# Optimization experiments

Hardware: AMD Instinct MI355X
Metric: run time of the kernel (lower is better)

## Reference

```python
import jax, jax.numpy as jnp
import numpy as np

B, N, M, R = 128, 511, 256, 64
IN = 512  # word_dim + tag_dim


def setup_inputs() -> dict:
    key = jax.random.key(0)
    ks = jax.random.split(key, 16)
    def w(k, shape, fan_in):
        return jax.random.normal(k, shape, dtype=jnp.float32) / np.sqrt(fan_in)
    inp = {
        "word_tag_emb": jax.random.normal(ks[0], (B, N, IN), dtype=jnp.float32),
        "rel_emb": jax.random.normal(ks[1], (B, N, R), dtype=jnp.float32),
        "n_nodes": N,
    }
    for j, nm in enumerate(["ix", "fx", "ux", "ox"]):
        inp["W" + nm] = w(ks[2 + j], (IN, M), IN)
        inp["b" + nm] = jnp.zeros((M,), jnp.float32)
    for j, nm in enumerate(["ih", "fh", "uh", "oh"]):
        inp["W" + nm] = w(ks[6 + j], (M, M), M)
        inp["b" + nm] = jnp.zeros((M,), jnp.float32)
    # seq_lstm (nn.LSTM, 1 layer): gate order i, f, g, o; stored [in, 4M]
    inp["W_seq_ih"] = w(ks[10], (M + R, 4 * M), M + R)
    inp["W_seq_hh"] = w(ks[11], (M, 4 * M), M)
    inp["b_seq_ih"] = jnp.zeros((4 * M,), jnp.float32)
    inp["b_seq_hh"] = jnp.zeros((4 * M,), jnp.float32)
    return inp


def reference(word_tag_emb, rel_emb,
              Wix, bix, Wfx, bfx, Wux, bux, Wox, box,
              Wih, bih, Wfh, bfh, Wuh, buh, Woh, boh,
              W_seq_ih, W_seq_hh, b_seq_ih, b_seq_hh, n_nodes):
    Bn, Nn, _ = word_tag_emb.shape
    Mm = Wih.shape[0]
    dt = word_tag_emb.dtype

    def lstm_cell(x, h, c):
        g = x @ W_seq_ih + h @ W_seq_hh + (b_seq_ih + b_seq_hh)
        i, f, gg, o = jnp.split(g, 4, axis=-1)
        c2 = jax.nn.sigmoid(f) * c + jax.nn.sigmoid(i) * jnp.tanh(gg)
        return jax.nn.sigmoid(o) * jnp.tanh(c2), c2

    def step(carry, node):
        h_buf, c_buf = carry  # [B, N, M] state buffers
        ch = jnp.stack([2 * node + 1, 2 * node + 2])        # heap children
        valid = (ch < Nn).astype(dt)[:, None, None]          # [2,1,1]
        idx = jnp.minimum(ch, Nn - 1)
        ch_h = jnp.take(h_buf, idx, axis=1).transpose(1, 0, 2) * valid   # [2,B,M]
        ch_c = jnp.take(c_buf, idx, axis=1).transpose(1, 0, 2) * valid   # [2,B,M]
        ch_r = jnp.take(rel_emb, idx, axis=1).transpose(1, 0, 2) * valid # [2,B,R]
        # seq_lstm over the (masked) child sequence: input [h_j ; rel_j]
        hs = jnp.zeros((Bn, Mm), dt)
        cs = jnp.zeros((Bn, Mm), dt)
        for j in range(2):  # fixed max_children (binary tree)
            hn, cn = lstm_cell(jnp.concatenate([ch_h[j], ch_r[j]], -1), hs, cs)
            hs = valid[j] * hn + (1.0 - valid[j]) * hs
            cs = valid[j] * cn + (1.0 - valid[j]) * cs
        h_tilde = hs  # stays zero at leaves (seq_lstm never run there)
        x = word_tag_emb[:, node]  # [B, IN]
        i = jax.nn.sigmoid(x @ Wix + bix + h_tilde @ Wih + bih)
        o = jax.nn.sigmoid(x @ Wox + box + h_tilde @ Woh + boh)
        u = jnp.tanh(x @ Wux + bux + h_tilde @ Wuh + buh)
        f = jax.nn.sigmoid((x @ Wfx + bfx)[None] + ch_h @ Wfh + bfh)  # [2,B,M]
        c = i * u + jnp.sum(f * ch_c * valid, axis=0)
        h = o * jnp.tanh(c)
        h_buf = h_buf.at[:, node].set(h)
        c_buf = c_buf.at[:, node].set(c)
        return (h_buf, c_buf), None

    h0 = jnp.zeros((Bn, Nn, Mm), dt)
    c0 = jnp.zeros((Bn, Nn, Mm), dt)
    nodes = jnp.arange(Nn - 1, -1, -1)  # bottom-up (children before parents)
    (h_buf, c_buf), _ = jax.lax.scan(step, (h0, c0), nodes)
    return h_buf[:, 0]  # root hidden state, [B, M]
```

## Files before the change

### kernel.cpp

```cpp
#include <hip/hip_runtime.h>
#include <math.h>

#define NNODE 511

typedef short s16x8 __attribute__((ext_vector_type(8)));
typedef float f32x4 __attribute__((ext_vector_type(4)));

__device__ __forceinline__ unsigned short f2bf(float f) {
  unsigned int u = __builtin_bit_cast(unsigned int, f);
  u += 0x7fffu + ((u >> 16) & 1u);
  return (unsigned short)(u >> 16);
}
__device__ __forceinline__ float sigf(float x) {
  float e = __builtin_amdgcn_exp2f(-1.442695040888963f * x);
  return __builtin_amdgcn_rcpf(1.0f + e);
}
__device__ __forceinline__ float tanh_a(float x) {
  float e = __builtin_amdgcn_exp2f(2.885390081777927f * x);
  return 1.0f - 2.0f * __builtin_amdgcn_rcpf(1.0f + e);
}

__device__ __forceinline__ void load16_lds(const unsigned short* g, unsigned short* l) {
  __builtin_amdgcn_global_load_lds(
      (const __attribute__((address_space(1))) void*)g,
      (__attribute__((address_space(3))) void*)l, 16, 0, 0);
}

template<int N> __device__ __forceinline__ void s_wait_vmcnt() {
  asm volatile("s_waitcnt vmcnt(%0)" :: "n"(N) : "memory");
}

__device__ __forceinline__ void swz_blk(int& bx, int& by) {
  bx = blockIdx.x; by = blockIdx.y;
  int ny = gridDim.y;
  if ((ny & 7) == 0) {
    int lin = by * 8 + bx;
    int w = lin >> 3;
    by = (lin & 7) * (ny >> 3) + (w >> 3);
    bx = w & 7;
  }
}

__global__ void k_prep_x(const float* __restrict__ w, unsigned short* __restrict__ xbf) {
  int o = (blockIdx.x * 256 + threadIdx.x) * 4;
  int node = o >> 16;
  int b = (o >> 9) & 127;
  int k = o & 511;
  const float4 v = *(const float4*)(w + ((size_t)b * NNODE + node) * 512 + k);
  unsigned int p0 = (unsigned int)f2bf(v.x) | ((unsigned int)f2bf(v.y) << 16);
  unsigned int p1 = (unsigned int)f2bf(v.z) | ((unsigned int)f2bf(v.w) << 16);
  *(uint2*)(xbf + o) = make_uint2(p0, p1);
}

__global__ void k_prep_w(const float* __restrict__ Wix, const float* __restrict__ Wux,
                         const float* __restrict__ Wox, const float* __restrict__ Wfx,
                         const float* __restrict__ Wih, const float* __restrict__ Wuh,
                         const float* __restrict__ Woh, const float* __restrict__ Wfh,
                         const float* __restrict__ Wsi, const float* __restrict__ Wsh,
                         unsigned short* __restrict__ WL2t, unsigned short* __restrict__ WA2t,
                         unsigned short* __restrict__ WH2t, unsigned short* __restrict__ WEX2t) {
  int idx = blockIdx.x * 256 + threadIdx.x;
  if (idx < 393216) {
    int c = idx >> 9, k = idx & 511;
    int G = c / 48, rem = c - G * 48, g = rem >> 4, mi = rem & 15, m = G * 16 + mi;
    const float* W = (g == 0) ? Wix : (g == 1) ? Wux : Wox;
    WL2t[idx] = f2bf(W[k * 256 + m]);
  } else if (idx < 802816) {
    int o = idx - 393216;
    int c = o / 320, k = o - c * 320;
    int G = c / 80, rem = c - G * 80, g = rem >> 4, mi = rem & 15, m = G * 16 + mi;
    float v;
    if (g < 4) v = Wsi[k * 1024 + g * 256 + m];
    else       v = (k < 256) ? Wfh[k * 256 + m] : 0.0f;
    WA2t[o] = f2bf(v);
  } else if (idx < 1064960) {
    int o = idx - 802816;
    int c = o >> 8, k = o & 255;
    int G = c >> 6, rem = c & 63, g = rem >> 4, mi = rem & 15, m = G * 16 + mi;
    WH2t[o] = f2bf(Wsh[k * 1024 + g * 256 + m]);
  } else if (idx < 1851392) {
    int o = idx - 1064960;
    int c = o / 768, k = o - c * 768;
    int G = c >> 6, rem = c & 63, g = rem >> 4, mi = rem & 15, m = G * 16 + mi;
    float v;
    if (k < 256) {
      v = (g == 0) ? Wih[k * 256 + m] : (g == 1) ? Wuh[k * 256 + m]
        : (g == 2) ? Woh[k * 256 + m] : 0.0f;
    } else {
      int k2 = k - 256;
      v = (g == 0) ? Wix[k2 * 256 + m] : (g == 1) ? Wux[k2 * 256 + m]
        : (g == 2) ? Wox[k2 * 256 + m] : Wfx[k2 * 256 + m];
    }
    WEX2t[o] = f2bf(v);
  }
}

#define MFMA_BODY(AP, BP, NG, CW)                                             \
  _Pragma("unroll")                                                           \
  for (int kk = 0; kk < 64; kk += 32) {                                       \
    const int sw = (kk | (q * 8)) ^ ((m16 & 7) * 8);                          \
    s16x8 af[4], bfr[NG];                                                     \
    _Pragma("unroll")                                                         \
    for (int i = 0; i < 4; ++i)                                               \
      af[i] = *(const s16x8*)(&(AP)[(wm + i * 16 + m16) * 64 + sw]);          \
    _Pragma("unroll")                                                         \
    for (int j = 0; j < NG; ++j)                                              \
      bfr[j] = *(const s16x8*)(&(BP)[(wc * CW + j * 16 + m16) * 64 + sw]);    \
    _Pragma("unroll")                                                         \
    for (int i = 0; i < 4; ++i)                                               \
      _Pragma("unroll")                                                       \
      for (int j = 0; j < NG; ++j)                                            \
        acc[i][j] = __builtin_amdgcn_mfma_f32_16x16x32_bf16(af[i], bfr[j], acc[i][j], 0, 0, 0); \
  }

#define STAGE(DST, SRC, STRIDE, R, K0)                                        \
  _Pragma("unroll")                                                           \
  for (int c = 0; c < (R) / 32; ++c) {                                        \
    int row8 = wave * ((R) / 4) + c * 8;                                      \
    load16_lds(SRC + (size_t)(row8 + l8) * (STRIDE) + (K0) + gsw, &(DST)[row8 * 64]); \
  }

#define STEP_SYNC(VM)                                                         \
  s_wait_vmcnt<VM>();                                                         \
  __builtin_amdgcn_s_barrier();                                               \
  __builtin_amdgcn_sched_barrier(0);

__global__ __launch_bounds__(256, 2) void k_gemm1(
    const unsigned short* __restrict__ AinL, const unsigned short* __restrict__ AinR,
    const unsigned short* __restrict__ Bt,
    unsigned short* __restrict__ h1, float* __restrict__ c1,
    float* __restrict__ FHL, float* __restrict__ FHR, float* __restrict__ PR,
    const float* __restrict__ bsi, const float* __restrict__ bsh, int crows) {
  __shared__ alignas(16) unsigned short As[2][128 * 64];
  __shared__ alignas(16) unsigned short Bs[2][160 * 64];
  int bx, by; swz_blk(bx, by);
  const int t = threadIdx.x;
  const int wave = t >> 6, lane = t & 63;
  const int wm = (wave & 1) * 64, wc = wave >> 1;
  const int m16 = lane & 15, q = lane >> 4;
  const int l8 = lane >> 3, l7 = lane & 7;
  const int gsw = ((l7 ^ l8) * 8);
  const int rowBase = by * 128;
  const bool isL = rowBase < crows;
  const unsigned short* Arow = isL ? (AinL + (size_t)rowBase * 320)
                                   : (AinR + (size_t)(rowBase - crows) * 320);
  const unsigned short* Brow = Bt + (size_t)bx * 160 * 320;
  f32x4 acc[4][5] = {};
  const int m = (bx * 2 + wc) * 16 + m16;

  float bi = 0.f, bg = 0.f, bo = 0.f;
  if (isL) {
    bi = bsi[m] + bsh[m];
    bg = bsi[512 + m] + bsh[512 + m];
    bo = bsi[768 + m] + bsh[768 + m];
  }

  STAGE(As[0], Arow, 320, 128, 0)
  STAGE(Bs[0], Brow, 320, 160, 0)
#pragma unroll
  for (int ti = 0; ti < 5; ++ti) {
    if (ti < 4) {
      STAGE(As[(ti + 1) & 1], Arow, 320, 128, (ti + 1) * 64)
      STAGE(Bs[(ti + 1) & 1], Brow, 320, 160, (ti + 1) * 64)
      STEP_SYNC(9)
    } else {
      STEP_SYNC(0)
    }
    MFMA_BODY(As[ti & 1], Bs[ti & 1], 5, 80)
    __builtin_amdgcn_s_barrier();
  }

  if (isL) {
#pragma unroll
    for (int i = 0; i < 4; ++i)
#pragma unroll
      for (int r2 = 0; r2 < 4; ++r2) {
        int r = rowBase + wm + i * 16 + q * 4 + r2;
        float ii = sigf(acc[i][0][r2] + bi);
        float gg = tanh_a(acc[i][2][r2] + bg);
        float oo = sigf(acc[i][3][r2] + bo);
        float cv = ii * gg;
        size_t o = (size_t)r * 256 + m;
        h1[o] = f2bf(oo * tanh_a(cv));
        c1[o] = cv;
        FHL[o] = acc[i][4][r2];
      }
  } else {
#pragma unroll
    for (int i = 0; i < 4; ++i)
#pragma unroll
      for (int r2 = 0; r2 < 4; ++r2) {
        int rr = rowBase - crows + wm + i * 16 + q * 4 + r2;
        size_t o = (size_t)rr * 256 + m;
        float4 pv = {acc[i][0][r2], acc[i][1][r2], acc[i][2][r2], acc[i][3][r2]};
        *(float4*)(PR + o * 4) = pv;
        FHR[o] = acc[i][4][r2];
      }
  }
}

__global__ __launch_bounds__(256, 2) void k_gemm2(
    const unsigned short* __restrict__ A, const unsigned short* __restrict__ Bt,
    const float* __restrict__ PR, const float* __restrict__ c1,
    unsigned short* __restrict__ HT,
    const float* __restrict__ bsi, const float* __restrict__ bsh) {
  __shared__ alignas(16) unsigned short As[2][128 * 64];
  __shared__ alignas(16) unsigned short Bs[2][128 * 64];
  int bx, by; swz_blk(bx, by);
  const int t = threadIdx.x;
  const int wave = t >> 6, lane = t & 63;
  const int wm = (wave & 1) * 64, wc = wave >> 1;
  const int m16 = lane & 15, q = lane >> 4;
  const int l8 = lane >> 3, l7 = lane & 7;
  const int gsw = ((l7 ^ l8) * 8);
  const int rowBase = by * 128;
  const unsigned short* Arow = A + (size_t)rowBase * 256;
  const unsigned short* Brow = Bt + (size_t)bx * 128 * 256;
  f32x4 acc[4][4] = {};
  const int m = (bx * 2 + wc) * 16 + m16;

  float b0 = bsi[m] + bsh[m];
  float b1 = bsi[256 + m] + bsh[256 + m];
  float b2 = bsi[512 + m] + bsh[512 + m];
  float b3 = bsi[768 + m] + bsh[768 + m];

  float4 ppr[4][4];
  float pc[4][4];

  STAGE(As[0], Arow, 256, 128, 0)
  STAGE(Bs[0], Brow, 256, 128, 0)
#pragma unroll
  for (int ti = 0; ti < 4; ++ti) {
    if (ti < 3) {
      STAGE(As[(ti + 1) & 1], Arow, 256, 128, (ti + 1) * 64)
      STAGE(Bs[(ti + 1) & 1], Brow, 256, 128, (ti + 1) * 64)
      STEP_SYNC(8)
      if (ti == 2) {
#pragma unroll
        for (int i = 0; i < 4; ++i)
#pragma unroll
          for (int r2 = 0; r2 < 4; ++r2) {
            int r = rowBase + wm + i * 16 + q * 4 + r2;
            size_t o = (size_t)r * 256 + m;
            ppr[i][r2] = *(const float4*)(PR + o * 4);
            pc[i][r2] = c1[o];
          }
      }
    } else {
      STEP_SYNC(32)
    }
    MFMA_BODY(As[ti & 1], Bs[ti & 1], 4, 64)
    __builtin_amdgcn_s_barrier();
  }

#pragma unroll
  for (int i = 0; i < 4; ++i)
#pragma unroll
    for (int r2 = 0; r2 < 4; ++r2) {
      int r = rowBase + wm + i * 16 + q * 4 + r2;
      size_t o = (size_t)r * 256 + m;
      float4 pv = ppr[i][r2];
      float ii = sigf(acc[i][0][r2] + pv.x + b0);
      float ff = sigf(acc[i][1][r2] + pv.y + b1);
      float gg = tanh_a(acc[i][2][r2] + pv.z + b2);
      float oo = sigf(acc[i][3][r2] + pv.w + b3);
      float c2 = ff * pc[i][r2] + ii * gg;
      HT[o] = f2bf(oo * tanh_a(c2));
    }
}

__global__ __launch_bounds__(256, 2) void k_gemm3(
    const unsigned short* __restrict__ HT, const unsigned short* __restrict__ xnode,
    const unsigned short* __restrict__ Bt,
    const float* __restrict__ FHL, const float* __restrict__ FHR,
    float* __restrict__ cbuf, unsigned short* __restrict__ Ain,
    const float* __restrict__ rel, float* __restrict__ out,
    const float* __restrict__ bix, const float* __restrict__ bih,
    const float* __restrict__ bux, const float* __restrict__ buh,
    const float* __restrict__ box, const float* __restrict__ boh,
    const float* __restrict__ bfx, const float* __restrict__ bfh,
    int base, int v0, int n, int lvl) {
  __shared__ alignas(16) unsigned short As[2][128 * 64];
  __shared__ alignas(16) unsigned short Bs[2][128 * 64];
  int bx, by; swz_blk(bx, by);
  const int t = threadIdx.x;
  const int wave = t >> 6, lane = t & 63;
  const int wm = (wave & 1) * 64, wc = wave >> 1;
  const int m16 = lane & 15, q = lane >> 4;
  const int l8 = lane >> 3, l7 = lane & 7;
  const int gsw = ((l7 ^ l8) * 8);
  const int rowBase = by * 128;
  const unsigned short* Brow = Bt + (size_t)bx * 128 * 768;
  f32x4 acc[4][4] = {};
  const int m = (bx * 2 + wc) * 16 + m16;

  float bi = bix[m] + bih[m];
  float bu = bux[m] + buh[m];
  float bo = box[m] + boh[m];
  float bf = bfx[m] + bfh[m];

  float pfl[4][4], pfr[4][4], pc0[4][4], pc1v[4][4];

  auto stageA = [&](unsigned short* dst, int kb) {
    if (kb < 256) {
      const unsigned short* Arow = HT + (size_t)rowBase * 256;
#pragma unroll
      for (int c = 0; c < 4; ++c) {
        int row8 = wave * 32 + c * 8;
        load16_lds(Arow + (size_t)(row8 + l8) * 256 + kb + gsw, &dst[row8 * 64]);
      }
    } else {
      const unsigned short* Arow = xnode + (size_t)rowBase * 512;
      int k0 = kb - 256;
#pragma unroll
      for (int c = 0; c < 4; ++c) {
        int row8 = wave * 32 + c * 8;
        load16_lds(Arow + (size_t)(row8 + l8) * 512 + k0 + gsw, &dst[row8 * 64]);
      }
    }
  };

  stageA(As[0], 0);
  STAGE(Bs[0], Brow, 768, 128, 0)
#pragma unroll
  for (int ti = 0; ti < 12; ++ti) {
    if (ti < 11) {
      stageA(As[(ti + 1) & 1], (ti + 1) * 64);
      STAGE(Bs[(ti + 1) & 1], Brow, 768, 128, (ti + 1) * 64)
      STEP_SYNC(8)
      if (ti == 10) {
#pragma unroll
        for (int i = 0; i < 4; ++i)
#pragma unroll
          for (int r2 = 0; r2 < 4; ++r2) {
            int r = rowBase + wm + i * 16 + q * 4 + r2;
            int b = r & 127;
            int node = base + v0 + (r >> 7);
            size_t o = (size_t)r * 256 + m;
            size_t co = ((size_t)(2 * node + 1) * 128 + b) * 256 + m;
            pfl[i][r2] = FHL[o];
            pfr[i][r2] = FHR[o];
            pc0[i][r2] = cbuf[co];
            pc1v[i][r2] = cbuf[co + 32768];
          }
      }
    } else {
      STEP_SYNC(63)
    }
    MFMA_BODY(As[ti & 1], Bs[ti & 1], 4, 64)
    __builtin_amdgcn_s_barrier();
  }

#pragma unroll
  for (int i = 0; i < 4; ++i)
#pragma unroll
    for (int r2 = 0; r2 < 4; ++r2) {
      int r = rowBase + wm + i * 16 + q * 4 + r2;
      int vloc = r >> 7, b = r & 127;
      int vg = v0 + vloc;
      int node = base + vg;
      size_t o = (size_t)r * 256 + m;
      float pf = acc[i][3][r2] + bf;
      float f0 = sigf(pf + pfl[i][r2]);
      float f1 = sigf(pf + pfr[i][r2]);
      float ii = sigf(acc[i][0][r2] + bi);
      float uu = tanh_a(acc[i][1][r2] + bu);
      float oo = sigf(acc[i][2][r2] + bo);
      float cc = ii * uu + f0 * pc0[i][r2] + f1 * pc1v[i][r2];
      float hh = oo * tanh_a(cc);
      if (lvl == 0) {
        out[b * 256 + m] = hh;
      } else {
        cbuf[((size_t)node * 128 + b) * 256 + m] = cc;
        int rowA = (vg & 1) * (n >> 1) * 128 + (vg >> 1) * 128 + b;
        Ain[(size_t)rowA * 320 + m] = f2bf(hh);
        if (m < 64)
          Ain[(size_t)rowA * 320 + 256 + m] = f2bf(rel[((size_t)b * NNODE + node) * 64 + m]);
      }
    }
}

__global__ __launch_bounds__(256, 2) void k_leaf(
    const unsigned short* __restrict__ xleaf, const unsigned short* __restrict__ Bt,
    float* __restrict__ cbuf, unsigned short* __restrict__ Ain,
    const float* __restrict__ rel,
    const float* __restrict__ bix, const float* __restrict__ bih,
    const float* __restrict__ bux, const float* __restrict__ buh,
    const float* __restrict__ box, const float* __restrict__ boh) {
  __shared__ alignas(16) unsigned short As[2][128 * 64];
  __shared__ alignas(16) unsigned short Bs[2][96 * 64];
  int bx, by; swz_blk(bx, by);
  const int t = threadIdx.x;
  const int wave = t >> 6, lane = t & 63;
  const int wm = (wave & 1) * 64, wc = wave >> 1;
  const int m16 = lane & 15, q = lane >> 4;
  const int l8 = lane >> 3, l7 = lane & 7;
  const int gsw = ((l7 ^ l8) * 8);
  const int rowBase = by * 128;
  const unsigned short* Arow = xleaf + (size_t)rowBase * 512;
  const unsigned short* Brow = Bt + (size_t)bx * 96 * 512;
  f32x4 acc[4][3] = {};
  const int m = (bx * 2 + wc) * 16 + m16;

  float bi = bix[m] + bih[m];
  float bu = bux[m] + buh[m];
  float bo = box[m] + boh[m];

  STAGE(As[0], Arow, 512, 128, 0)
#pragma unroll
  for (int c = 0; c < 3; ++c) {
    int row8 = wave * 24 + c * 8;
    load16_lds(Brow + (size_t)(row8 + l8) * 512 + 0 + gsw, &Bs[0][row8 * 64]);
  }
#pragma unroll
  for (int ti = 0; ti < 8; ++ti) {
    if (ti < 7) {
      int kn = (ti + 1) * 64;
      STAGE(As[(ti + 1) & 1], Arow, 512, 128, kn)
#pragma unroll
      for (int c = 0; c < 3; ++c) {
        int row8 = wave * 24 + c * 8;
        load16_lds(Brow + (size_t)(row8 + l8) * 512 + kn + gsw, &Bs[(ti + 1) & 1][row8 * 64]);
      }
      STEP_SYNC(7)
    } else {
      STEP_SYNC(0)
    }
    MFMA_BODY(As[ti & 1], Bs[ti & 1], 3, 48)
    __builtin_amdgcn_s_barrier();
  }

#pragma unroll
  for (int i = 0; i < 4; ++i)
#pragma unroll
    for (int r2 = 0; r2 < 4; ++r2) {
      int r = rowBase + wm + i * 16 + q * 4 + r2;
      int vg = r >> 7, b = r & 127;
      int node = 255 + vg;
      float ii = sigf(acc[i][0][r2] + bi);
      float uu = tanh_a(acc[i][1][r2] + bu);
      float oo = sigf(acc[i][2][r2] + bo);
      float cc = ii * uu;
      float hh = oo * tanh_a(cc);
      cbuf[((size_t)node * 128 + b) * 256 + m] = cc;
      int rowA = (vg & 1) * 16384 + (vg >> 1) * 128 + b;
      Ain[(size_t)rowA * 320 + m] = f2bf(hh);
      if (m < 64)
        Ain[(size_t)rowA * 320 + 256 + m] = f2bf(rel[((size_t)b * NNODE + node) * 64 + m]);
    }
}

extern "C" void kernel_launch(void* const* d_in, const int* in_sizes, int n_in,
                              void* d_out, int out_size, void* d_ws, size_t ws_size,
                              hipStream_t stream) {
  const float* wte = (const float*)d_in[0];
  const float* rel = (const float*)d_in[1];
  const float* Wix = (const float*)d_in[3];
  const float* bix = (const float*)d_in[4];
  const float* Wfx = (const float*)d_in[5];
  const float* bfx = (const float*)d_in[6];
  const float* Wux = (const float*)d_in[7];
  const float* bux = (const float*)d_in[8];
  const float* Wox = (const float*)d_in[9];
  const float* box = (const float*)d_in[10];
  const float* Wih = (const float*)d_in[11];
  const float* bih = (const float*)d_in[12];
  const float* Wfh = (const float*)d_in[13];
  const float* bfh = (const float*)d_in[14];
  const float* Wuh = (const float*)d_in[15];
  const float* buh = (const float*)d_in[16];
  const float* Woh = (const float*)d_in[17];
  const float* boh = (const float*)d_in[18];
  const float* Wsi = (const float*)d_in[19];
  const float* Wsh = (const float*)d_in[20];
  const float* bsi = (const float*)d_in[21];
  const float* bsh = (const float*)d_in[22];
  float* out = (float*)d_out;
  (void)in_sizes; (void)n_in; (void)out_size;

  int INT_MAXN;
  if (ws_size >= (size_t)310 * 1024 * 1024)      INT_MAXN = 128;
  else if (ws_size >= (size_t)200 * 1024 * 1024) INT_MAXN = 32;
  else                                           INT_MAXN = 8;
  const int crowsMax = INT_MAXN * 128;

  char* ws = (char*)d_ws;
  size_t off = 0;
  auto alloc = [&](size_t bytes) {
    size_t o = off; off += (bytes + 255) & ~(size_t)255; return o;
  };
  unsigned short* xbf  = (unsigned short*)(ws + alloc((size_t)NNODE * 128 * 512 * 2));
  float*          cbuf = (float*)         (ws + alloc((size_t)NNODE * 128 * 256 * 4));
  unsigned short* Ain  = (unsigned short*)(ws + alloc((size_t)32768 * 320 * 2));
  unsigned short* WL2t = (unsigned short*)(ws + alloc((size_t)768 * 512 * 2));
  unsigned short* WA2t = (unsigned short*)(ws + alloc((size_t)1280 * 320 * 2));
  unsigned short* WH2t = (unsigned short*)(ws + alloc((size_t)1024 * 256 * 2));
  unsigned short* WEX2t= (unsigned short*)(ws + alloc((size_t)1024 * 768 * 2));
  unsigned short* h1   = (unsigned short*)(ws + alloc((size_t)crowsMax * 256 * 2));
  float*          c1   = (float*)         (ws + alloc((size_t)crowsMax * 256 * 4));
  float*          FHL  = (float*)         (ws + alloc((size_t)crowsMax * 256 * 4));
  float*          FHR  = (float*)         (ws + alloc((size_t)crowsMax * 256 * 4));
  float*          PR   = (float*)         (ws + alloc((size_t)crowsMax * 1024 * 4));
  unsigned short* HT   = (unsigned short*)(ws + alloc((size_t)crowsMax * 256 * 2));

  k_prep_x<<<32704, 256, 0, stream>>>(wte, xbf);
  k_prep_w<<<7232, 256, 0, stream>>>(Wix, Wux, Wox, Wfx, Wih, Wuh, Woh, Wfh,
                                     Wsi, Wsh, WL2t, WA2t, WH2t, WEX2t);

  k_leaf<<<dim3(8, 256), 256, 0, stream>>>(xbf + (size_t)255 * 128 * 512, WL2t,
                                           cbuf, Ain, rel, bix, bih, bux, buh, box, boh);

  for (int lvl = 7; lvl >= 0; --lvl) {
    int n = 1 << lvl;
    int base = n - 1;
    int cn = (n < INT_MAXN) ? n : INT_MAXN;
    for (int v0 = 0; v0 < n; v0 += cn) {
      int crows = cn * 128;
      const unsigned short* AinL = Ain + (size_t)(v0 * 128) * 320;
      const unsigned short* AinR = Ain + (size_t)((n + v0) * 128) * 320;
      const unsigned short* xnode = xbf + (size_t)(base + v0) * 128 * 512;
      k_gemm1<<<dim3(8, 2 * cn), 256, 0, stream>>>(AinL, AinR, WA2t, h1, c1,
                                                   FHL, FHR, PR, bsi, bsh, crows);
      k_gemm2<<<dim3(8, cn), 256, 0, stream>>>(h1, WH2t, PR, c1, HT, bsi, bsh);
      k_gemm3<<<dim3(8, cn), 256, 0, stream>>>(HT, xnode, WEX2t, FHL, FHR, cbuf, Ain,
                                               rel, out, bix, bih, bux, buh, box, boh,
                                               bfx, bfh, base, v0, n, lvl);
    }
  }
}
```

Baseline: 745.0 us.

## Move right-child input GEMM into gemm2 via concatenated K, dropping PR buffer

The right child's input projection (x_r @ W_seq_ih) and its Wfh product no longer run in gemm1 with their pre-activations written to a PR buffer. gemm2 now concatenates h1 with the right child's input along K (576) against a combined weight matrix, producing the second LSTM step's gates and FHR directly. This removes the float4 PR write and read round trip and halves the gemm1 grid. In exchange gemm2 does a longer K loop with a wider B tile, and weight prep grows.

```diff
diff --git a/kernel.cpp b/kernel.cpp
--- a/kernel.cpp
+++ b/kernel.cpp
@@ -58,7 +58,7 @@
                          const float* __restrict__ Woh, const float* __restrict__ Wfh,
                          const float* __restrict__ Wsi, const float* __restrict__ Wsh,
                          unsigned short* __restrict__ WL2t, unsigned short* __restrict__ WA2t,
-                         unsigned short* __restrict__ WH2t, unsigned short* __restrict__ WEX2t) {
+                         unsigned short* __restrict__ WG2t, unsigned short* __restrict__ WEX2t) {
   int idx = blockIdx.x * 256 + threadIdx.x;
   if (idx < 393216) {
     int c = idx >> 9, k = idx & 511;
@@ -73,13 +73,17 @@
     if (g < 4) v = Wsi[k * 1024 + g * 256 + m];
     else       v = (k < 256) ? Wfh[k * 256 + m] : 0.0f;
     WA2t[o] = f2bf(v);
-  } else if (idx < 1064960) {
+  } else if (idx < 1540096) {
     int o = idx - 802816;
-    int c = o >> 8, k = o & 255;
-    int G = c >> 6, rem = c & 63, g = rem >> 4, mi = rem & 15, m = G * 16 + mi;
-    WH2t[o] = f2bf(Wsh[k * 1024 + g * 256 + m]);
-  } else if (idx < 1851392) {
-    int o = idx - 1064960;
+    int c = o / 576, k = o - c * 576;
+    int G = c / 80, rem = c - G * 80, g = rem >> 4, mi = rem & 15, m = G * 16 + mi;
+    float v;
+    if (g < 4) v = (k < 256) ? Wsh[k * 1024 + g * 256 + m]
+                             : Wsi[(k - 256) * 1024 + g * 256 + m];
+    else       v = (k >= 256 && k < 512) ? Wfh[(k - 256) * 256 + m] : 0.0f;
+    WG2t[o] = f2bf(v);
+  } else if (idx < 2326528) {
+    int o = idx - 1540096;
     int c = o / 768, k = o - c * 768;
     int G = c >> 6, rem = c & 63, g = rem >> 4, mi = rem & 15, m = G * 16 + mi;
     float v;
@@ -126,11 +130,10 @@
   __builtin_amdgcn_sched_barrier(0);
 
 __global__ __launch_bounds__(256, 2) void k_gemm1(
-    const unsigned short* __restrict__ AinL, const unsigned short* __restrict__ AinR,
-    const unsigned short* __restrict__ Bt,
+    const unsigned short* __restrict__ AinL, const unsigned short* __restrict__ Bt,
     unsigned short* __restrict__ h1, float* __restrict__ c1,
-    float* __restrict__ FHL, float* __restrict__ FHR, float* __restrict__ PR,
-    const float* __restrict__ bsi, const float* __restrict__ bsh, int crows) {
+    float* __restrict__ FHL,
+    const float* __restrict__ bsi, const float* __restrict__ bsh) {
   __shared__ alignas(16) unsigned short As[2][128 * 64];
   __shared__ alignas(16) unsigned short Bs[2][160 * 64];
   int bx, by; swz_blk(bx, by);
@@ -141,19 +144,14 @@
   const int l8 = lane >> 3, l7 = lane & 7;
   const int gsw = ((l7 ^ l8) * 8);
   const int rowBase = by * 128;
-  const bool isL = rowBase < crows;
-  const unsigned short* Arow = isL ? (AinL + (size_t)rowBase * 320)
-                                   : (AinR + (size_t)(rowBase - crows) * 320);
+  const unsigned short* Arow = AinL + (size_t)rowBase * 320;
   const unsigned short* Brow = Bt + (size_t)bx * 160 * 320;
   f32x4 acc[4][5] = {};
   const int m = (bx * 2 + wc) * 16 + m16;
 
-  float bi = 0.f, bg = 0.f, bo = 0.f;
-  if (isL) {
-    bi = bsi[m] + bsh[m];
-    bg = bsi[512 + m] + bsh[512 + m];
-    bo = bsi[768 + m] + bsh[768 + m];
-  }
+  float bi = bsi[m] + bsh[m];
+  float bg = bsi[512 + m] + bsh[512 + m];
+  float bo = bsi[768 + m] + bsh[768 + m];
 
   STAGE(As[0], Arow, 320, 128, 0)
   STAGE(Bs[0], Brow, 320, 160, 0)
@@ -170,42 +168,30 @@
     __builtin_amdgcn_s_barrier();
   }
 
-  if (isL) {
-#pragma unroll
-    for (int i = 0; i < 4; ++i)
-#pragma unroll
-      for (int r2 = 0; r2 < 4; ++r2) {
-        int r = rowBase + wm + i * 16 + q * 4 + r2;
-        float ii = sigf(acc[i][0][r2] + bi);
-        float gg = tanh_a(acc[i][2][r2] + bg);
-        float oo = sigf(acc[i][3][r2] + bo);
-        float cv = ii * gg;
-        size_t o = (size_t)r * 256 + m;
-        h1[o] = f2bf(oo * tanh_a(cv));
-        c1[o] = cv;
-        FHL[o] = acc[i][4][r2];
-      }
-  } else {
-#pragma unroll
-    for (int i = 0; i < 4; ++i)
-#pragma unroll
-      for (int r2 = 0; r2 < 4; ++r2) {
-        int rr = rowBase - crows + wm + i * 16 + q * 4 + r2;
-        size_t o = (size_t)rr * 256 + m;
-        float4 pv = {acc[i][0][r2], acc[i][1][r2], acc[i][2][r2], acc[i][3][r2]};
-        *(float4*)(PR + o * 4) = pv;
-        FHR[o] = acc[i][4][r2];
-      }
-  }
+#pragma unroll
+  for (int i = 0; i < 4; ++i)
+#pragma unroll
+    for (int r2 = 0; r2 < 4; ++r2) {
+      int r = rowBase + wm + i * 16 + q * 4 + r2;
+      float ii = sigf(acc[i][0][r2] + bi);
+      float gg = tanh_a(acc[i][2][r2] + bg);
+      float oo = sigf(acc[i][3][r2] + bo);
+      float cv = ii * gg;
+      size_t o = (size_t)r * 256 + m;
+      h1[o] = f2bf(oo * tanh_a(cv));
+      c1[o] = cv;
+      FHL[o] = acc[i][4][r2];
+    }
 }
 
 __global__ __launch_bounds__(256, 2) void k_gemm2(
-    const unsigned short* __restrict__ A, const unsigned short* __restrict__ Bt,
-    const float* __restrict__ PR, const float* __restrict__ c1,
-    unsigned short* __restrict__ HT,
+    const unsigned short* __restrict__ h1, const unsigned short* __restrict__ AinR,
+    const unsigned short* __restrict__ Bt,
+    const float* __restrict__ c1, unsigned short* __restrict__ HT,
+    float* __restrict__ FHR,
     const float* __restrict__ bsi, const float* __restrict__ bsh) {
   __shared__ alignas(16) unsigned short As[2][128 * 64];
-  __shared__ alignas(16) unsigned short Bs[2][128 * 64];
+  __shared__ alignas(16) unsigned short Bs[2][160 * 64];
   int bx, by; swz_blk(bx, by);
   const int t = threadIdx.x;
   const int wave = t >> 6, lane = t & 63;
@@ -214,9 +200,8 @@
   const int l8 = lane >> 3, l7 = lane & 7;
   const int gsw = ((l7 ^ l8) * 8);
   const int rowBase = by * 128;
-  const unsigned short* Arow = A + (size_t)rowBase * 256;
-  const unsigned short* Brow = Bt + (size_t)bx * 128 * 256;
-  f32x4 acc[4][4] = {};
+  const unsigned short* Brow = Bt + (size_t)bx * 160 * 576;
+  f32x4 acc[4][5] = {};
   const int m = (bx * 2 + wc) * 16 + m16;
 
   float b0 = bsi[m] + bsh[m];
@@ -224,32 +209,48 @@
   float b2 = bsi[512 + m] + bsh[512 + m];
   float b3 = bsi[768 + m] + bsh[768 + m];
 
-  float4 ppr[4][4];
   float pc[4][4];
 
-  STAGE(As[0], Arow, 256, 128, 0)
-  STAGE(Bs[0], Brow, 256, 128, 0)
-#pragma unroll
-  for (int ti = 0; ti < 4; ++ti) {
-    if (ti < 3) {
-      STAGE(As[(ti + 1) & 1], Arow, 256, 128, (ti + 1) * 64)
-      STAGE(Bs[(ti + 1) & 1], Brow, 256, 128, (ti + 1) * 64)
-      STEP_SYNC(8)
-      if (ti == 2) {
+  auto stageA = [&](unsigned short* dst, int kb) {
+    if (kb < 256) {
+      const unsigned short* Arow = h1 + (size_t)rowBase * 256;
+#pragma unroll
+      for (int c = 0; c < 4; ++c) {
+        int row8 = wave * 32 + c * 8;
+        load16_lds(Arow + (size_t)(row8 + l8) * 256 + kb + gsw, &dst[row8 * 64]);
+      }
+    } else {
+      const unsigned short* Arow = AinR + (size_t)rowBase * 320;
+      int k0 = kb - 256;
+#pragma unroll
+      for (int c = 0; c < 4; ++c) {
+        int row8 = wave * 32 + c * 8;
+        load16_lds(Arow + (size_t)(row8 + l8) * 320 + k0 + gsw, &dst[row8 * 64]);
+      }
+    }
+  };
+
+  stageA(As[0], 0);
+  STAGE(Bs[0], Brow, 576, 160, 0)
+#pragma unroll
+  for (int ti = 0; ti < 9; ++ti) {
+    if (ti < 8) {
+      stageA(As[(ti + 1) & 1], (ti + 1) * 64);
+      STAGE(Bs[(ti + 1) & 1], Brow, 576, 160, (ti + 1) * 64)
+      STEP_SYNC(9)
+      if (ti == 7) {
 #pragma unroll
         for (int i = 0; i < 4; ++i)
 #pragma unroll
           for (int r2 = 0; r2 < 4; ++r2) {
             int r = rowBase + wm + i * 16 + q * 4 + r2;
-            size_t o = (size_t)r * 256 + m;
-            ppr[i][r2] = *(const float4*)(PR + o * 4);
-            pc[i][r2] = c1[o];
+            pc[i][r2] = c1[(size_t)r * 256 + m];
           }
       }
     } else {
-      STEP_SYNC(32)
-    }
-    MFMA_BODY(As[ti & 1], Bs[ti & 1], 4, 64)
+      STEP_SYNC(16)
+    }
+    MFMA_BODY(As[ti & 1], Bs[ti & 1], 5, 80)
     __builtin_amdgcn_s_barrier();
   }
 
@@ -259,13 +260,13 @@
     for (int r2 = 0; r2 < 4; ++r2) {
       int r = rowBase + wm + i * 16 + q * 4 + r2;
       size_t o = (size_t)r * 256 + m;
-      float4 pv = ppr[i][r2];
-      float ii = sigf(acc[i][0][r2] + pv.x + b0);
-      float ff = sigf(acc[i][1][r2] + pv.y + b1);
-      float gg = tanh_a(acc[i][2][r2] + pv.z + b2);
-      float oo = sigf(acc[i][3][r2] + pv.w + b3);
+      float ii = sigf(acc[i][0][r2] + b0);
+      float ff = sigf(acc[i][1][r2] + b1);
+      float gg = tanh_a(acc[i][2][r2] + b2);
+      float oo = sigf(acc[i][3][r2] + b3);
       float c2 = ff * pc[i][r2] + ii * gg;
       HT[o] = f2bf(oo * tanh_a(c2));
+      FHR[o] = acc[i][4][r2];
     }
 }
 
@@ -359,7 +360,6 @@
       int vloc = r >> 7, b = r & 127;
       int vg = v0 + vloc;
       int node = base + vg;
-      size_t o = (size_t)r * 256 + m;
       float pf = acc[i][3][r2] + bf;
       float f0 = sigf(pf + pfl[i][r2]);
       float f1 = sigf(pf + pfr[i][r2]);
@@ -494,18 +494,17 @@
   unsigned short* Ain  = (unsigned short*)(ws + alloc((size_t)32768 * 320 * 2));
   unsigned short* WL2t = (unsigned short*)(ws + alloc((size_t)768 * 512 * 2));
   unsigned short* WA2t = (unsigned short*)(ws + alloc((size_t)1280 * 320 * 2));
-  unsigned short* WH2t = (unsigned short*)(ws + alloc((size_t)1024 * 256 * 2));
+  unsigned short* WG2t = (unsigned short*)(ws + alloc((size_t)1280 * 576 * 2));
   unsigned short* WEX2t= (unsigned short*)(ws + alloc((size_t)1024 * 768 * 2));
   unsigned short* h1   = (unsigned short*)(ws + alloc((size_t)crowsMax * 256 * 2));
   float*          c1   = (float*)         (ws + alloc((size_t)crowsMax * 256 * 4));
   float*          FHL  = (float*)         (ws + alloc((size_t)crowsMax * 256 * 4));
   float*          FHR  = (float*)         (ws + alloc((size_t)crowsMax * 256 * 4));
-  float*          PR   = (float*)         (ws + alloc((size_t)crowsMax * 1024 * 4));
   unsigned short* HT   = (unsigned short*)(ws + alloc((size_t)crowsMax * 256 * 2));
 
   k_prep_x<<<32704, 256, 0, stream>>>(wte, xbf);
-  k_prep_w<<<7232, 256, 0, stream>>>(Wix, Wux, Wox, Wfx, Wih, Wuh, Woh, Wfh,
-                                     Wsi, Wsh, WL2t, WA2t, WH2t, WEX2t);
+  k_prep_w<<<9088, 256, 0, stream>>>(Wix, Wux, Wox, Wfx, Wih, Wuh, Woh, Wfh,
+                                     Wsi, Wsh, WL2t, WA2t, WG2t, WEX2t);
 
   k_leaf<<<dim3(8, 256), 256, 0, stream>>>(xbf + (size_t)255 * 128 * 512, WL2t,
                                            cbuf, Ain, rel, bix, bih, bux, buh, box, boh);
@@ -515,13 +514,11 @@
     int base = n - 1;
     int cn = (n < INT_MAXN) ? n : INT_MAXN;
     for (int v0 = 0; v0 < n; v0 += cn) {
-      int crows = cn * 128;
       const unsigned short* AinL = Ain + (size_t)(v0 * 128) * 320;
       const unsigned short* AinR = Ain + (size_t)((n + v0) * 128) * 320;
       const unsigned short* xnode = xbf + (size_t)(base + v0) * 128 * 512;
-      k_gemm1<<<dim3(8, 2 * cn), 256, 0, stream>>>(AinL, AinR, WA2t, h1, c1,
-                                                   FHL, FHR, PR, bsi, bsh, crows);
-      k_gemm2<<<dim3(8, cn), 256, 0, stream>>>(h1, WH2t, PR, c1, HT, bsi, bsh);
+      k_gemm1<<<dim3(8, cn), 256, 0, stream>>>(AinL, WA2t, h1, c1, FHL, bsi, bsh);
+      k_gemm2<<<dim3(8, cn), 256, 0, stream>>>(h1, AinR, WG2t, c1, HT, FHR, bsi, bsh);
       k_gemm3<<<dim3(8, cn), 256, 0, stream>>>(HT, xnode, WEX2t, FHL, FHR, cbuf, Ain,
                                                rel, out, bix, bih, bux, buh, box, boh,
                                                bfx, bfh, base, v0, n, lvl);
```

New measurement: 742.5 us. No clear change (-0.3%).
